# Performance work log

Hardware: AMD Instinct MI355X
Metric: run time of the kernel (lower is better)

Reference implementation:

```python
import jax, jax.numpy as jnp
import numpy as np

B, T, C, H = 2, 2048, 1024, 16
D = C // H  # d_head = 64


def setup_inputs() -> dict:
    key = jax.random.key(0)
    k1, k2, k3 = jax.random.split(key, 3)
    x = jax.random.normal(k1, (B, T, C), dtype=jnp.float32)
    # torch Linear weights stored pre-transposed as [in, out] so we apply x @ W
    w_qkv = jax.random.normal(k2, (C, 3 * C), dtype=jnp.float32) * (C ** -0.5)
    w_out = jax.random.normal(k3, (C, C), dtype=jnp.float32) * (C ** -0.5)
    charge_w = jnp.array([0.0, 3.0, 6.0], dtype=jnp.float32)  # CHARGES init
    # causal mask, broadcast over batch and heads; mask==0 positions are blocked
    mask = jnp.tril(jnp.ones((1, 1, T, T), dtype=jnp.int32))
    return {"x": x, "mask": mask, "w_qkv": w_qkv, "w_out": w_out, "charge_w": charge_w}


def reference(x, mask, w_qkv, w_out, charge_w):
    B, T, C = x.shape
    H = 16
    D = C // H
    qkv = (x @ w_qkv).reshape(B, T, 3, H, D)
    q, k, v = qkv[:, :, 0], qkv[:, :, 1], qkv[:, :, 2]  # each [B,T,H,D]
    scale = D ** -0.5
    attn = jnp.einsum("bqhd,bkhd->bhqk", q, k) * scale  # [B,H,T,T]
    charge_bias = jnp.mod(jnp.sum(charge_w), 9.0) * 0.001  # scalar bias
    attn = attn + charge_bias
    attn = jnp.where(mask == 0, jnp.float32(-1e9), attn)
    attn = jax.nn.softmax(attn, axis=-1)  # dropout is identity in eval mode
    out = jnp.einsum("bhqk,bkhd->bqhd", attn, v).reshape(B, T, C)
    return out @ w_out
```

## Files before the change

kernel.cpp:

```cpp
#include <hip/hip_runtime.h>
#include <stdint.h>


typedef __attribute__((ext_vector_type(4))) float f32x4;
typedef __attribute__((ext_vector_type(16))) float f32x16;
typedef __attribute__((ext_vector_type(8))) __bf16 bf16x8;
typedef __attribute__((ext_vector_type(8))) unsigned short ushort8;
typedef __attribute__((ext_vector_type(4))) unsigned short ushort4v;
typedef __attribute__((ext_vector_type(4))) unsigned int uint4v;

#define DEV __device__ __forceinline__

DEV unsigned short f32_to_bf16(float f) {
    union { float f; unsigned int u; } cv; cv.f = f;
    unsigned int u = cv.u;
    return (unsigned short)((u + 0x7FFFu + ((u >> 16) & 1u)) >> 16);
}

DEV bf16x8 load_bf16x8(const unsigned short* p) {
    ushort8 v = *(const ushort8*)p;
    return __builtin_bit_cast(bf16x8, v);
}

DEV unsigned cvt_pk_bf16(float lo, float hi) {
    unsigned r;
    asm("v_cvt_pk_bf16_f32 %0, %1, %2" : "=v"(r) : "v"(lo), "v"(hi));
    return r;
}

DEV void gload_lds16(const void* g, void* l) {
    __builtin_amdgcn_global_load_lds(
        (const __attribute__((address_space(1))) unsigned int*)g,
        (__attribute__((address_space(3))) unsigned int*)l, 16, 0, 0);
}

DEV f32x16 vzero16() {
    f32x16 v;
#pragma unroll
    for (int i = 0; i < 16; ++i) v[i] = 0.f;
    return v;
}

DEV float tmax32(const f32x16& a, const f32x16& b) {
    float m[16];
#pragma unroll
    for (int i = 0; i < 16; ++i) m[i] = fmaxf(a[i], b[i]);
#pragma unroll
    for (int st = 8; st > 0; st >>= 1)
#pragma unroll
        for (int i = 0; i < 8; ++i) if (i < st) m[i] = fmaxf(m[i], m[i + st]);
    return m[0];
}
DEV float tsum32(const f32x16& a, const f32x16& b) {
    float m[16];
#pragma unroll
    for (int i = 0; i < 16; ++i) m[i] = a[i] + b[i];
#pragma unroll
    for (int st = 8; st > 0; st >>= 1)
#pragma unroll
        for (int i = 0; i < 8; ++i) if (i < st) m[i] = m[i] + m[i + st];
    return m[0];
}

__global__ void cvt_kernel(const float* __restrict__ in, unsigned short* __restrict__ out, int n) {
    int i = (blockIdx.x * blockDim.x + threadIdx.x) * 4;
    if (i >= n) return;
    f32x4 v = *(const f32x4*)(in + i);
    ushort4v o;
    o[0] = f32_to_bf16(v[0]); o[1] = f32_to_bf16(v[1]);
    o[2] = f32_to_bf16(v[2]); o[3] = f32_to_bf16(v[3]);
    *(ushort4v*)(out + i) = o;
}

__global__ __launch_bounds__(256) void tcvt_kernel(const float* __restrict__ in,
                                                   unsigned short* __restrict__ out,
                                                   int R, int Cn) {
    __shared__ float tl[32][33];
    const int tx = threadIdx.x & 31, ty = threadIdx.x >> 5;
    const int c0 = blockIdx.x * 32, r0 = blockIdx.y * 32;
#pragma unroll
    for (int rr = 0; rr < 4; ++rr) {
        int r = ty + rr * 8;
        tl[r][tx] = in[(size_t)(r0 + r) * Cn + c0 + tx];
    }
    __syncthreads();
#pragma unroll
    for (int rr = 0; rr < 4; ++rr) {
        int cc = ty + rr * 8;
        out[(size_t)(c0 + cc) * R + r0 + tx] = f32_to_bf16(tl[tx][cc]);
    }
}

template<bool OUT_BF16, bool SCALE_Q>
__global__ __launch_bounds__(256) void gemm_kernel(
    const unsigned short* __restrict__ A,
    const unsigned short* __restrict__ Bt,
    void* __restrict__ C, int K, int ldc)
{
    __shared__ __align__(16) unsigned short As[2][4096];
    __shared__ __align__(16) unsigned short Bs[2][4096];

    const int tid = threadIdx.x;
    const int lane = tid & 63;
    const int w = tid >> 6;
    const int wr = w >> 1, wc = w & 1;
    const int g = lane >> 4, ci = lane & 15;
    const int bx = blockIdx.x, by = blockIdx.y;
    const int soff = w * 1024 + lane * 16;
    const int srow = soff >> 6;
    const int scch = (soff >> 4) & 3;

#define GSTAGE(buf, k0_) do { \
    _Pragma("unroll") for (int i_ = 0; i_ < 2; ++i_) { \
        int row_ = srow + i_ * 64; \
        gload_lds16(A  + (size_t)(by * 128 + row_) * K + (k0_) + scch * 8, \
                    (char*)As[buf] + i_ * 4096 + w * 1024); \
        gload_lds16(Bt + (size_t)(bx * 128 + row_) * K + (k0_) + scch * 8, \
                    (char*)Bs[buf] + i_ * 4096 + w * 1024); } } while (0)

    f32x4 acc[4][4];
#pragma unroll
    for (int i = 0; i < 4; ++i)
#pragma unroll
        for (int j = 0; j < 4; ++j) acc[i][j] = f32x4{0.f, 0.f, 0.f, 0.f};

    GSTAGE(0, 0);
    asm volatile("s_waitcnt vmcnt(0)" ::: "memory");
    __builtin_amdgcn_sched_barrier(0);
    __builtin_amdgcn_s_barrier();
    __builtin_amdgcn_sched_barrier(0);

    const int nk = K >> 5;
    for (int kt = 0; kt < nk; ++kt) {
        const int cur = kt & 1;
        if (kt + 1 < nk) GSTAGE(cur ^ 1, (kt + 1) << 5);

        bf16x8 af[4], bfr[4];
#pragma unroll
        for (int mf = 0; mf < 4; ++mf) af[mf]  = load_bf16x8(&As[cur][(wr * 64 + mf * 16 + ci) * 32 + g * 8]);
#pragma unroll
        for (int nf = 0; nf < 4; ++nf) bfr[nf] = load_bf16x8(&Bs[cur][(wc * 64 + nf * 16 + ci) * 32 + g * 8]);
#pragma unroll
        for (int mf = 0; mf < 4; ++mf)
#pragma unroll
            for (int nf = 0; nf < 4; ++nf)
                acc[mf][nf] = __builtin_amdgcn_mfma_f32_16x16x32_bf16(af[mf], bfr[nf], acc[mf][nf], 0, 0, 0);

        asm volatile("s_waitcnt vmcnt(0) lgkmcnt(0)" ::: "memory");
        __builtin_amdgcn_sched_barrier(0);
        __builtin_amdgcn_s_barrier();
        __builtin_amdgcn_sched_barrier(0);
    }
#undef GSTAGE

#pragma unroll
    for (int mf = 0; mf < 4; ++mf)
#pragma unroll
        for (int nf = 0; nf < 4; ++nf)
#pragma unroll
            for (int r = 0; r < 4; ++r) {
                int row = by * 128 + wr * 64 + mf * 16 + g * 4 + r;
                int col = bx * 128 + wc * 64 + nf * 16 + ci;
                float v = acc[mf][nf][r];
                if (SCALE_Q && col < 1024) v *= 0.1803368801f;
                if (OUT_BF16)
                    ((unsigned short*)C)[(size_t)row * ldc + col] = f32_to_bf16(v);
                else
                    ((float*)C)[(size_t)row * ldc + col] = v;
            }
}

__global__ __launch_bounds__(256) void attn4_kernel(const unsigned short* __restrict__ qkv,
                                                    unsigned short* __restrict__ attn) {
    constexpr int T = 2048, HD3 = 3072, Cc = 1024;
    __shared__ __align__(16) unsigned short Ks[3][4096];
    __shared__ __align__(16) unsigned short Vt[2][4096];

    const int tid = threadIdx.x;
    const int lane = tid & 63;
    const int w = tid >> 6;
    const int l31 = lane & 31;
    const int hi = lane >> 5;

    const int bx = blockIdx.x;
    const int qb = (bx < 256) ? (15 - (bx >> 5)) : ((bx - 256) >> 5);
    const int bh = bx & 31;
    const int h = bh & 15;
    const int b = bh >> 4;
    const int q0w = qb * 128 + w * 32;
    const int qrow = q0w + l31;
    const size_t base = (size_t)b * T * HD3;

    bf16x8 qf[4];
#pragma unroll
    for (int t = 0; t < 4; ++t)
        qf[t] = load_bf16x8(qkv + base + (size_t)qrow * HD3 + h * 64 + t * 16 + hi * 8);

    f32x16 acc0 = vzero16(), acc1 = vzero16();
    float m = -3e38f, l = 0.f;
    const int nt = 2 * qb + 2;

    ushort8 vA0, vA1, vB0, vB1;
#define LOADV(tile, r0, r1) do { int kv0_ = (tile) * 64; \
    int rr0_ = tid >> 3, cc0_ = tid & 7; \
    r0 = *(const ushort8*)(qkv + base + (size_t)(kv0_ + rr0_) * HD3 + 2 * Cc + h * 64 + cc0_ * 8); \
    int c1_ = 256 + tid; int rr1_ = c1_ >> 3, cc1_ = c1_ & 7; \
    r1 = *(const ushort8*)(qkv + base + (size_t)(kv0_ + rr1_) * HD3 + 2 * Cc + h * 64 + cc1_ * 8); } while (0)

#define DMAK(tile, kb) do { int kv0_ = (tile) * 64; \
    _Pragma("unroll") for (int i_ = 0; i_ < 2; ++i_) { \
        int off_ = i_ * 4096 + w * 1024 + lane * 16; \
        int row_ = off_ >> 7; \
        int csw_ = ((lane & 7) * 8) ^ ((row_ & 7) * 8); \
        gload_lds16(qkv + base + (size_t)(kv0_ + row_) * HD3 + Cc + h * 64 + csw_, \
                    (void*)(((char*)&Ks[kb][0]) + i_ * 4096 + w * 1024)); } } while (0)

#define WRITEV(vb, r0, r1) do { \
    _Pragma("unroll") for (int i_ = 0; i_ < 2; ++i_) { \
        int c_ = i_ * 256 + tid; int row_ = c_ >> 3, cc_ = c_ & 7; \
        ushort8 v_ = i_ ? r1 : r0; \
        _Pragma("unroll") for (int j_ = 0; j_ < 8; ++j_) { \
            int d_ = cc_ * 8 + j_; \
            int sw_ = ((d_ ^ (d_ >> 3)) & 7) * 8; \
            Vt[vb][d_ * 64 + (row_ ^ sw_)] = v_[j_]; } } } while (0)

    LOADV(0, vA0, vA1);
    DMAK(0, 0);
    asm volatile("s_waitcnt vmcnt(0)" ::: "memory");
    __builtin_amdgcn_sched_barrier(0);
    WRITEV(0, vA0, vA1);
    LOADV(1, vB0, vB1);
    DMAK(1, 1);
    asm volatile("s_waitcnt lgkmcnt(0)" ::: "memory");
    __builtin_amdgcn_sched_barrier(0);
    __builtin_amdgcn_s_barrier();
    __builtin_amdgcn_sched_barrier(0);

    for (int t = 0; t < nt; ++t) {
        const int kv0 = t * 64;
        const int kcur = t % 3;
        const int vcur = t & 1;
        const bool act = (kv0 <= q0w + 31);
        const bool pre2 = (t + 2) < nt;

        if (t + 1 < nt) {
            if (t & 1) WRITEV(vcur ^ 1, vA0, vA1); else WRITEV(vcur ^ 1, vB0, vB1);
        }
        if (pre2) {
            if (t & 1) LOADV(t + 2, vB0, vB1); else LOADV(t + 2, vA0, vA1);
            DMAK(t + 2, (t + 2) % 3);
        }

        if (act) {
            f32x16 s0 = vzero16(), s1 = vzero16();
            bf16x8 pf[4];
            const bool st1_ok = (kv0 + 32 <= q0w + 31);
            __builtin_amdgcn_s_setprio(1);
#pragma unroll
            for (int tt = 0; tt < 4; ++tt) {
                int row = l31;
                int idx = kcur * 4096 + row * 64 + ((tt * 16 + hi * 8) ^ ((row & 7) * 8));
                s0 = __builtin_amdgcn_mfma_f32_32x32x16_bf16(load_bf16x8(&Ks[0][idx]), qf[tt], s0, 0, 0, 0);
            }
            if (st1_ok) {
#pragma unroll
                for (int tt = 0; tt < 4; ++tt) {
                    int row = 32 + l31;
                    int idx = kcur * 4096 + row * 64 + ((tt * 16 + hi * 8) ^ ((row & 7) * 8));
                    s1 = __builtin_amdgcn_mfma_f32_32x32x16_bf16(load_bf16x8(&Ks[0][idx]), qf[tt], s1, 0, 0, 0);
                }
            }
            __builtin_amdgcn_s_setprio(0);
            const bool needmask = (kv0 + 63 > q0w);
            if (needmask) {
#pragma unroll
                for (int G = 0; G < 4; ++G)
#pragma unroll
                    for (int rr = 0; rr < 4; ++rr) {
                        int kvb = kv0 + 8 * G + 4 * hi + rr;
                        s0[G * 4 + rr] = (kvb      <= qrow) ? s0[G * 4 + rr] : -3e38f;
                        s1[G * 4 + rr] = (kvb + 32 <= qrow) ? s1[G * 4 + rr] : -3e38f;
                    }
            }
            float pmax = tmax32(s0, s1);
            pmax = fmaxf(pmax, __shfl_xor(pmax, 32));
            if (!__all(pmax - m <= 11.5f)) {
                float mnew = fmaxf(m, pmax);
                float alpha = exp2f(m - mnew);
                m = mnew;
                l *= alpha;
#pragma unroll
                for (int i = 0; i < 16; ++i) { acc0[i] *= alpha; acc1[i] *= alpha; }
            }
#pragma unroll
            for (int i = 0; i < 16; ++i) {
                s0[i] = exp2f(s0[i] - m);
                s1[i] = exp2f(s1[i] - m);
            }

            unsigned pk0[4][2], pk1[4][2];
#pragma unroll
            for (int G = 0; G < 4; ++G) {
                pk0[G][0] = cvt_pk_bf16(s0[G * 4 + 0], s0[G * 4 + 1]);
                pk0[G][1] = cvt_pk_bf16(s0[G * 4 + 2], s0[G * 4 + 3]);
                pk1[G][0] = cvt_pk_bf16(s1[G * 4 + 0], s1[G * 4 + 1]);
                pk1[G][1] = cvt_pk_bf16(s1[G * 4 + 2], s1[G * 4 + 3]);
            }
#pragma unroll
            for (int tf = 0; tf < 4; ++tf) {
                const int kb = tf & 1;
                unsigned sA0, sA1, sB0, sB1;
                if (tf < 2) { sA0 = pk0[2 * kb][0]; sA1 = pk0[2 * kb][1]; sB0 = pk0[2 * kb + 1][0]; sB1 = pk0[2 * kb + 1][1]; }
                else        { sA0 = pk1[2 * kb][0]; sA1 = pk1[2 * kb][1]; sB0 = pk1[2 * kb + 1][0]; sB1 = pk1[2 * kb + 1][1]; }
                unsigned sd0 = hi ? sA0 : sB0, sd1 = hi ? sA1 : sB1;
                unsigned rc0 = (unsigned)__shfl_xor((int)sd0, 32);
                unsigned rc1 = (unsigned)__shfl_xor((int)sd1, 32);
                uint4v u;
                u[0] = hi ? rc0 : sA0;  u[1] = hi ? rc1 : sA1;
                u[2] = hi ? sB0 : rc0;  u[3] = hi ? sB1 : rc1;
                pf[tf] = __builtin_bit_cast(bf16x8, u);
            }

            __builtin_amdgcn_s_setprio(1);
#pragma unroll
            for (int tt = 0; tt < 4; ++tt) {
                {
                    int d = l31, sw = ((d ^ (d >> 3)) & 7) * 8;
                    bf16x8 vf = load_bf16x8(&Vt[vcur][d * 64 + ((tt * 16 + hi * 8) ^ sw)]);
                    acc0 = __builtin_amdgcn_mfma_f32_32x32x16_bf16(vf, pf[tt], acc0, 0, 0, 0);
                }
                {
                    int d = 32 + l31, sw = ((d ^ (d >> 3)) & 7) * 8;
                    bf16x8 vf = load_bf16x8(&Vt[vcur][d * 64 + ((tt * 16 + hi * 8) ^ sw)]);
                    acc1 = __builtin_amdgcn_mfma_f32_32x32x16_bf16(vf, pf[tt], acc1, 0, 0, 0);
                }
            }
            __builtin_amdgcn_s_setprio(0);

            float rsum = tsum32(s0, s1);
            l += rsum + __shfl_xor(rsum, 32);
        }

        if (pre2) asm volatile("s_waitcnt vmcnt(4) lgkmcnt(0)" ::: "memory");
        else      asm volatile("s_waitcnt vmcnt(0) lgkmcnt(0)" ::: "memory");
        __builtin_amdgcn_sched_barrier(0);
        __builtin_amdgcn_s_barrier();
        __builtin_amdgcn_sched_barrier(0);
    }

    const float invl = 1.0f / l;
    const size_t ob = (size_t)b * T * Cc + (size_t)qrow * Cc + h * 64;
#pragma unroll
    for (int G = 0; G < 4; ++G) {
        ushort4v o0, o1;
#pragma unroll
        for (int rr = 0; rr < 4; ++rr) {
            o0[rr] = f32_to_bf16(acc0[G * 4 + rr] * invl);
            o1[rr] = f32_to_bf16(acc1[G * 4 + rr] * invl);
        }
        int d0 = 8 * G + 4 * hi;
        *(ushort4v*)(attn + ob + d0) = o0;
        *(ushort4v*)(attn + ob + 32 + d0) = o1;
    }
#undef LOADV
#undef DMAK
#undef WRITEV
}

extern "C" void kernel_launch(void* const* d_in, const int* in_sizes, int n_in,
                              void* d_out, int out_size, void* d_ws, size_t ws_size,
                              hipStream_t stream) {
    const float* x     = (const float*)d_in[0];
    const float* w_qkv = (const float*)d_in[2];
    const float* w_out = (const float*)d_in[3];
    float* out = (float*)d_out;

    unsigned short* xb     = (unsigned short*)d_ws;
    unsigned short* wqkvT  = xb + 4194304;
    unsigned short* woutT  = wqkvT + 3145728;
    unsigned short* qkv    = woutT + 1048576;
    unsigned short* attn   = qkv + 12582912;

    cvt_kernel<<<4096, 256, 0, stream>>>(x, xb, 4194304);
    tcvt_kernel<<<dim3(96, 32), 256, 0, stream>>>(w_qkv, wqkvT, 1024, 3072);
    tcvt_kernel<<<dim3(32, 32), 256, 0, stream>>>(w_out, woutT, 1024, 1024);

    gemm_kernel<true, true><<<dim3(24, 32), 256, 0, stream>>>(xb, wqkvT, (void*)qkv, 1024, 3072);

    attn4_kernel<<<512, 256, 0, stream>>>(qkv, attn);

    gemm_kernel<false, false><<<dim3(8, 32), 256, 0, stream>>>(attn, woutT, (void*)out, 1024, 1024);
}
```

Baseline: 156.0 us.

## Split long causal attention query blocks across two KV chunks with combine pass

Query blocks 8-15 now have their key/value range split into two halves, each handled by its own workgroup. Each half writes unnormalized bf16 partial outputs plus running max and sum to scratch space that reuses the x and weight buffers. A new combine kernel merges the two halves with the usual log-sum-exp rescaling. The aim is to balance work across 768 workgroups and shorten the critical path set by the longest causal blocks, at the cost of an extra launch, extra scratch traffic, and bf16 rounding of the partial results.

```diff
diff --git a/kernel.cpp b/kernel.cpp
--- a/kernel.cpp
+++ b/kernel.cpp
@@ -17,6 +17,11 @@
     return (unsigned short)((u + 0x7FFFu + ((u >> 16) & 1u)) >> 16);
 }
 
+DEV float bf16_to_f32(unsigned short u) {
+    union { unsigned int i; float f; } cv; cv.i = ((unsigned int)u) << 16;
+    return cv.f;
+}
+
 DEV bf16x8 load_bf16x8(const unsigned short* p) {
     ushort8 v = *(const ushort8*)p;
     return __builtin_bit_cast(bf16x8, v);
@@ -61,6 +66,9 @@
         for (int i = 0; i < 8; ++i) if (i < st) m[i] = m[i] + m[i + st];
     return m[0];
 }
+
+__device__ __constant__ unsigned char qtab[24] = {15,15,7,14,14,13,13,6,12,12,11,11,5,10,10,9,9,4,8,8,3,2,1,0};
+__device__ __constant__ unsigned char ctab[24] = {0,1,255,0,1,0,1,255,0,1,0,1,255,0,1,0,1,255,0,1,255,255,255,255};
 
 __global__ void cvt_kernel(const float* __restrict__ in, unsigned short* __restrict__ out, int n) {
     int i = (blockIdx.x * blockDim.x + threadIdx.x) * 4;
@@ -170,8 +178,10 @@
             }
 }
 
-__global__ __launch_bounds__(256) void attn4_kernel(const unsigned short* __restrict__ qkv,
-                                                    unsigned short* __restrict__ attn) {
+__global__ __launch_bounds__(256) void attn5_kernel(const unsigned short* __restrict__ qkv,
+                                                    unsigned short* __restrict__ attn,
+                                                    unsigned short* __restrict__ Obuf,
+                                                    float* __restrict__ mlbuf) {
     constexpr int T = 2048, HD3 = 3072, Cc = 1024;
     __shared__ __align__(16) unsigned short Ks[3][4096];
     __shared__ __align__(16) unsigned short Vt[2][4096];
@@ -183,14 +193,21 @@
     const int hi = lane >> 5;
 
     const int bx = blockIdx.x;
-    const int qb = (bx < 256) ? (15 - (bx >> 5)) : ((bx - 256) >> 5);
+    const int j = bx >> 5;
     const int bh = bx & 31;
+    const int q = qtab[j];
+    const int ct = ctab[j];
     const int h = bh & 15;
     const int b = bh >> 4;
-    const int q0w = qb * 128 + w * 32;
+    const int q0w = q * 128 + w * 32;
     const int qrow = q0w + l31;
     const size_t base = (size_t)b * T * HD3;
 
+    const int nt_full = 2 * q + 2;
+    const int ts = (ct == 1) ? (q + 1) : 0;
+    const int te = (ct == 0) ? (q + 1) : nt_full;
+    const int ntc = te - ts;
+
     bf16x8 qf[4];
 #pragma unroll
     for (int t = 0; t < 4; ++t)
@@ -198,7 +215,6 @@
 
     f32x16 acc0 = vzero16(), acc1 = vzero16();
     float m = -3e38f, l = 0.f;
-    const int nt = 2 * qb + 2;
 
     ushort8 vA0, vA1, vB0, vB1;
 #define LOADV(tile, r0, r1) do { int kv0_ = (tile) * 64; \
@@ -224,31 +240,32 @@
             int sw_ = ((d_ ^ (d_ >> 3)) & 7) * 8; \
             Vt[vb][d_ * 64 + (row_ ^ sw_)] = v_[j_]; } } } while (0)
 
-    LOADV(0, vA0, vA1);
-    DMAK(0, 0);
+    LOADV(ts, vA0, vA1);
+    DMAK(ts, 0);
     asm volatile("s_waitcnt vmcnt(0)" ::: "memory");
     __builtin_amdgcn_sched_barrier(0);
     WRITEV(0, vA0, vA1);
-    LOADV(1, vB0, vB1);
-    DMAK(1, 1);
+    LOADV(ts + 1, vB0, vB1);
+    DMAK(ts + 1, 1);
     asm volatile("s_waitcnt lgkmcnt(0)" ::: "memory");
     __builtin_amdgcn_sched_barrier(0);
     __builtin_amdgcn_s_barrier();
     __builtin_amdgcn_sched_barrier(0);
 
-    for (int t = 0; t < nt; ++t) {
+    for (int tt = 0; tt < ntc; ++tt) {
+        const int t = ts + tt;
         const int kv0 = t * 64;
-        const int kcur = t % 3;
-        const int vcur = t & 1;
+        const int kcur = tt % 3;
+        const int vcur = tt & 1;
         const bool act = (kv0 <= q0w + 31);
-        const bool pre2 = (t + 2) < nt;
-
-        if (t + 1 < nt) {
-            if (t & 1) WRITEV(vcur ^ 1, vA0, vA1); else WRITEV(vcur ^ 1, vB0, vB1);
+        const bool pre2 = (tt + 2) < ntc;
+
+        if (tt + 1 < ntc) {
+            if (tt & 1) WRITEV(vcur ^ 1, vA0, vA1); else WRITEV(vcur ^ 1, vB0, vB1);
         }
         if (pre2) {
-            if (t & 1) LOADV(t + 2, vB0, vB1); else LOADV(t + 2, vA0, vA1);
-            DMAK(t + 2, (t + 2) % 3);
+            if (tt & 1) LOADV(t + 2, vB0, vB1); else LOADV(t + 2, vA0, vA1);
+            DMAK(t + 2, (tt + 2) % 3);
         }
 
         if (act) {
@@ -257,17 +274,17 @@
             const bool st1_ok = (kv0 + 32 <= q0w + 31);
             __builtin_amdgcn_s_setprio(1);
 #pragma unroll
-            for (int tt = 0; tt < 4; ++tt) {
+            for (int tf = 0; tf < 4; ++tf) {
                 int row = l31;
-                int idx = kcur * 4096 + row * 64 + ((tt * 16 + hi * 8) ^ ((row & 7) * 8));
-                s0 = __builtin_amdgcn_mfma_f32_32x32x16_bf16(load_bf16x8(&Ks[0][idx]), qf[tt], s0, 0, 0, 0);
+                int idx = kcur * 4096 + row * 64 + ((tf * 16 + hi * 8) ^ ((row & 7) * 8));
+                s0 = __builtin_amdgcn_mfma_f32_32x32x16_bf16(load_bf16x8(&Ks[0][idx]), qf[tf], s0, 0, 0, 0);
             }
             if (st1_ok) {
 #pragma unroll
-                for (int tt = 0; tt < 4; ++tt) {
+                for (int tf = 0; tf < 4; ++tf) {
                     int row = 32 + l31;
-                    int idx = kcur * 4096 + row * 64 + ((tt * 16 + hi * 8) ^ ((row & 7) * 8));
-                    s1 = __builtin_amdgcn_mfma_f32_32x32x16_bf16(load_bf16x8(&Ks[0][idx]), qf[tt], s1, 0, 0, 0);
+                    int idx = kcur * 4096 + row * 64 + ((tf * 16 + hi * 8) ^ ((row & 7) * 8));
+                    s1 = __builtin_amdgcn_mfma_f32_32x32x16_bf16(load_bf16x8(&Ks[0][idx]), qf[tf], s1, 0, 0, 0);
                 }
             }
             __builtin_amdgcn_s_setprio(0);
@@ -323,16 +340,16 @@
 
             __builtin_amdgcn_s_setprio(1);
 #pragma unroll
-            for (int tt = 0; tt < 4; ++tt) {
+            for (int tf = 0; tf < 4; ++tf) {
                 {
                     int d = l31, sw = ((d ^ (d >> 3)) & 7) * 8;
-                    bf16x8 vf = load_bf16x8(&Vt[vcur][d * 64 + ((tt * 16 + hi * 8) ^ sw)]);
-                    acc0 = __builtin_amdgcn_mfma_f32_32x32x16_bf16(vf, pf[tt], acc0, 0, 0, 0);
+                    bf16x8 vf = load_bf16x8(&Vt[vcur][d * 64 + ((tf * 16 + hi * 8) ^ sw)]);
+                    acc0 = __builtin_amdgcn_mfma_f32_32x32x16_bf16(vf, pf[tf], acc0, 0, 0, 0);
                 }
                 {
                     int d = 32 + l31, sw = ((d ^ (d >> 3)) & 7) * 8;
-                    bf16x8 vf = load_bf16x8(&Vt[vcur][d * 64 + ((tt * 16 + hi * 8) ^ sw)]);
-                    acc1 = __builtin_amdgcn_mfma_f32_32x32x16_bf16(vf, pf[tt], acc1, 0, 0, 0);
+                    bf16x8 vf = load_bf16x8(&Vt[vcur][d * 64 + ((tf * 16 + hi * 8) ^ sw)]);
+                    acc1 = __builtin_amdgcn_mfma_f32_32x32x16_bf16(vf, pf[tf], acc1, 0, 0, 0);
                 }
             }
             __builtin_amdgcn_s_setprio(0);
@@ -348,23 +365,78 @@
         __builtin_amdgcn_sched_barrier(0);
     }
 
-    const float invl = 1.0f / l;
-    const size_t ob = (size_t)b * T * Cc + (size_t)qrow * Cc + h * 64;
-#pragma unroll
-    for (int G = 0; G < 4; ++G) {
-        ushort4v o0, o1;
-#pragma unroll
-        for (int rr = 0; rr < 4; ++rr) {
-            o0[rr] = f32_to_bf16(acc0[G * 4 + rr] * invl);
-            o1[rr] = f32_to_bf16(acc1[G * 4 + rr] * invl);
-        }
-        int d0 = 8 * G + 4 * hi;
-        *(ushort4v*)(attn + ob + d0) = o0;
-        *(ushort4v*)(attn + ob + 32 + d0) = o1;
+    if (ct == 255) {
+        const float invl = 1.0f / l;
+        const size_t ob = (size_t)b * T * Cc + (size_t)qrow * Cc + h * 64;
+#pragma unroll
+        for (int G = 0; G < 4; ++G) {
+            ushort4v o0, o1;
+#pragma unroll
+            for (int rr = 0; rr < 4; ++rr) {
+                o0[rr] = f32_to_bf16(acc0[G * 4 + rr] * invl);
+                o1[rr] = f32_to_bf16(acc1[G * 4 + rr] * invl);
+            }
+            int d0 = 8 * G + 4 * hi;
+            *(ushort4v*)(attn + ob + d0) = o0;
+            *(ushort4v*)(attn + ob + 32 + d0) = o1;
+        }
+    } else {
+        const int slot = bh * 16 + (q - 8) * 2 + ct;
+        const int qlocal = w * 32 + l31;
+        unsigned short* op = Obuf + (size_t)slot * 8192 + qlocal * 64;
+#pragma unroll
+        for (int G = 0; G < 4; ++G) {
+            ushort4v o0, o1;
+#pragma unroll
+            for (int rr = 0; rr < 4; ++rr) {
+                o0[rr] = f32_to_bf16(acc0[G * 4 + rr]);
+                o1[rr] = f32_to_bf16(acc1[G * 4 + rr]);
+            }
+            int d0 = 8 * G + 4 * hi;
+            *(ushort4v*)(op + d0) = o0;
+            *(ushort4v*)(op + 32 + d0) = o1;
+        }
+        if (hi == 0) {
+            mlbuf[slot * 256 + qlocal * 2]     = m;
+            mlbuf[slot * 256 + qlocal * 2 + 1] = l;
+        }
     }
 #undef LOADV
 #undef DMAK
 #undef WRITEV
+}
+
+__global__ __launch_bounds__(256) void combine_kernel(const unsigned short* __restrict__ Obuf,
+                                                      const float* __restrict__ mlbuf,
+                                                      unsigned short* __restrict__ attn) {
+    constexpr int T = 2048, Cc = 1024;
+    const int ss = blockIdx.x;
+    const int bh = ss >> 3, qq = 8 + (ss & 7);
+    const int b = bh >> 4, h = bh & 15;
+    const int slot0 = bh * 16 + (qq - 8) * 2;
+    const int tid = threadIdx.x;
+    const int qlocal = tid >> 1, dh = (tid & 1) * 32;
+
+    const float* ml0 = mlbuf + (size_t)slot0 * 256 + qlocal * 2;
+    const float* ml1 = ml0 + 256;
+    float m0 = ml0[0], l0 = ml0[1], m1 = ml1[0], l1 = ml1[1];
+    float M = fmaxf(m0, m1);
+    float w0 = exp2f(m0 - M), w1 = exp2f(m1 - M);
+    float inv = 1.f / (w0 * l0 + w1 * l1);
+
+    const unsigned short* p0 = Obuf + (size_t)slot0 * 8192 + qlocal * 64 + dh;
+    const unsigned short* p1 = p0 + 8192;
+    unsigned short* po = attn + (size_t)b * T * Cc + (size_t)(qq * 128 + qlocal) * Cc + h * 64 + dh;
+#pragma unroll
+    for (int i = 0; i < 4; ++i) {
+        ushort8 a = *(const ushort8*)(p0 + i * 8);
+        ushort8 c = *(const ushort8*)(p1 + i * 8);
+        ushort8 o;
+#pragma unroll
+        for (int k = 0; k < 8; ++k)
+            o[k] = f32_to_bf16((w0 * bf16_to_f32(a[k]) + w1 * bf16_to_f32(c[k])) * inv);
+        *(ushort8*)(po + i * 8) = o;
+    }
 }
 
 extern "C" void kernel_launch(void* const* d_in, const int* in_sizes, int n_in,
@@ -380,6 +452,8 @@
     unsigned short* woutT  = wqkvT + 3145728;
     unsigned short* qkv    = woutT + 1048576;
     unsigned short* attn   = qkv + 12582912;
+    unsigned short* Obuf   = xb;
+    float*          mlbuf  = (float*)wqkvT;
 
     cvt_kernel<<<4096, 256, 0, stream>>>(x, xb, 4194304);
     tcvt_kernel<<<dim3(96, 32), 256, 0, stream>>>(w_qkv, wqkvT, 1024, 3072);
@@ -387,7 +461,8 @@
 
     gemm_kernel<true, true><<<dim3(24, 32), 256, 0, stream>>>(xb, wqkvT, (void*)qkv, 1024, 3072);
 
-    attn4_kernel<<<512, 256, 0, stream>>>(qkv, attn);
+    attn5_kernel<<<768, 256, 0, stream>>>(qkv, attn, Obuf, mlbuf);
+    combine_kernel<<<256, 256, 0, stream>>>(Obuf, mlbuf, attn);
 
     gemm_kernel<false, false><<<dim3(8, 32), 256, 0, stream>>>(attn, woutT, (void*)out, 1024, 1024);
 }
```

New measurement: 139.8 us. 10.4% less time.
